# Kernel optimization log

Measured on AMD Instinct MI355X. Metric: run time of the kernel, lower is better.

The kernel has to match this reference:

```python
import jax, jax.numpy as jnp
import numpy as np

VTH = 1.0      # v_threshold
TAU = 2.0      # spikingjelly LIFNode default tau
ALPHA = 2.0    # ATan surrogate alpha
EPS = 1e-5     # BatchNorm eps
N_HEADS = 8
TOPK = 4       # routed regions per query region
REGION = 64    # tokens per region (4096 tokens -> 64 regions)


@jax.custom_vjp
def spike_fn(v):
    return (v >= VTH).astype(v.dtype)

def _spike_fwd(v):
    return (v >= VTH).astype(v.dtype), v

def _spike_bwd(v, g):
    sg = (ALPHA / 2.0) / (1.0 + (jnp.pi / 2.0 * ALPHA * (v - VTH)) ** 2)
    return (g * sg,)

spike_fn.defvjp(_spike_fwd, _spike_bwd)


def lif(x):
    # x: [T, B, L, D]; LIF with decay_input=True, hard reset to 0, detach_reset
    def step(v, xt):
        v = v + (xt - v) / TAU
        s = spike_fn(v)
        v = v * (1.0 - jax.lax.stop_gradient(s))
        return v, s
    _, s = jax.lax.scan(step, jnp.zeros_like(x[0]), x)
    return s


def batchnorm(x, gamma, beta):
    # torch BN1d over [T*B, D, L] in training mode == per-channel stats over (T,B,L)
    mean = x.mean(axis=(0, 1, 2))
    var = jnp.mean((x - mean) ** 2, axis=(0, 1, 2))
    return (x - mean) * jax.lax.rsqrt(var + EPS) * gamma + beta


def bilevel_attn(x, qkv_w, qkv_b, proj_w, proj_b):
    # x: [TB, L, D]
    TB, L, D = x.shape
    nreg = L // REGION
    hd = D // N_HEADS
    qkv = x @ qkv_w.T + qkv_b
    q, k, v = jnp.split(qkv, 3, axis=-1)
    qr = q.reshape(TB, nreg, REGION, D)
    kr = k.reshape(TB, nreg, REGION, D)
    vr = v.reshape(TB, nreg, REGION, D)
    # coarse region-level routing via mean-pooled q/k affinity
    aff = jnp.einsum('bnd,bmd->bnm', qr.mean(2), kr.mean(2))  # [TB, nreg, nreg]
    _, idx = jax.lax.top_k(aff, TOPK)                         # [TB, nreg, TOPK]
    gather = jax.vmap(lambda t, ix: t[ix])                    # per-sample region gather
    kg = gather(kr, idx).reshape(TB, nreg, TOPK * REGION, N_HEADS, hd)
    vg = gather(vr, idx).reshape(TB, nreg, TOPK * REGION, N_HEADS, hd)
    qh = qr.reshape(TB, nreg, REGION, N_HEADS, hd)
    logits = jnp.einsum('bnqhd,bnkhd->bnhqk', qh, kg) * (hd ** -0.5)
    p = jax.nn.softmax(logits, axis=-1)
    o = jnp.einsum('bnhqk,bnkhd->bnqhd', p, vg).reshape(TB, L, D)
    return o @ proj_w.T + proj_b


def setup_inputs() -> dict:
    key = jax.random.key(0)
    ks = jax.random.split(key, 8)
    T, B, Lt, L, D = 4, 2, 4, 1024, 256
    Ltot = Lt * L
    s = 0.02
    return {
        'x': jax.random.normal(ks[0], (T, B, Ltot, D), jnp.float32),
        'bn1_g': jnp.ones((D,), jnp.float32),
        'bn1_b': jnp.zeros((D,), jnp.float32),
        'bn2_g': jnp.ones((D,), jnp.float32),
        'bn2_b': jnp.zeros((D,), jnp.float32),
        'qkv_w': jax.random.normal(ks[1], (3 * D, D), jnp.float32) * s,
        'qkv_b': jnp.zeros((3 * D,), jnp.float32),
        'proj_w': jax.random.normal(ks[2], (D, D), jnp.float32) * s,
        'proj_b': jnp.zeros((D,), jnp.float32),
        'ffn_w1': jax.random.normal(ks[3], (4 * D, D), jnp.float32) * s,
        'ffn_b1': jnp.zeros((4 * D,), jnp.float32),
        'ffn_w2': jax.random.normal(ks[4], (D, 4 * D), jnp.float32) * s,
        'ffn_b2': jnp.zeros((D,), jnp.float32),
        'scale': jnp.ones((1,), jnp.float32) * 0.5,
        'Lt': Lt, 'b': B, 'L': L, 'dim': D,
    }


def reference(x, bn1_g, bn1_b, bn2_g, bn2_b, qkv_w, qkv_b, proj_w, proj_b,
              ffn_w1, ffn_b1, ffn_w2, ffn_b2, scale, Lt, b, L, dim):
    T = x.shape[0]
    Ltot = Lt * L
    # attention branch
    identity = x
    s1 = lif(batchnorm(x, bn1_g, bn1_b))
    a = bilevel_attn(s1.reshape(T * b, Ltot, dim), qkv_w, qkv_b, proj_w, proj_b)
    x = identity + a.reshape(T, b, Ltot, dim) * scale
    # ffn branch
    s2 = lif(batchnorm(x, bn2_g, bn2_b))
    h = jax.nn.gelu(s2 @ ffn_w1.T + ffn_b1, approximate=False) @ ffn_w2.T + ffn_b2
    return x + h * scale
```

## Files before the change

kernel.cpp:

```cpp
#include <hip/hip_runtime.h>
#include <hip/hip_bf16.h>
#include <math.h>

typedef __attribute__((ext_vector_type(8))) short short8;
typedef __attribute__((ext_vector_type(4))) float f32x4;

#define DIM 256
#define NROWS 32768
#define PERT 2097152
#define SAMP_TOK 4096

__device__ __forceinline__ float b2f(__hip_bfloat16 h){ return __bfloat162float(h); }
__device__ __forceinline__ __hip_bfloat16 f2b(float f){ return __float2bfloat16(f); }
__device__ __forceinline__ unsigned short f2bu(float f){
  __hip_bfloat16 h = __float2bfloat16(f);
  unsigned short u; __builtin_memcpy(&u, &h, 2); return u;
}

__global__ void f2b_k(const float* __restrict__ in, __hip_bfloat16* __restrict__ out, int n){
  int i = blockIdx.x * 256 + threadIdx.x;
  if (i < n) out[i] = f2b(in[i]);
}

__global__ void bn_stats_k(const float* __restrict__ x, float* __restrict__ sum, float* __restrict__ sumsq){
  int c = threadIdx.x;
  size_t base = (size_t)blockIdx.x * 256 * DIM + c;
  float s = 0.f, s2 = 0.f;
  for (int i = 0; i < 256; ++i){
    float v = x[base + (size_t)i * DIM];
    s += v; s2 += v * v;
  }
  atomicAdd(&sum[c], s);
  atomicAdd(&sumsq[c], s2);
}

__global__ void bn_fin_k(const float* __restrict__ sum, const float* __restrict__ sumsq,
                         const float* __restrict__ g, const float* __restrict__ b,
                         float* __restrict__ a_out, float* __restrict__ b_out){
  int c = threadIdx.x;
  float mean = sum[c] * (1.f/32768.f);
  float var  = sumsq[c] * (1.f/32768.f) - mean*mean;
  float a = g[c] / sqrtf(var + 1e-5f);
  a_out[c] = a;
  b_out[c] = b[c] - mean * a;
}

__global__ void lif_k(const float* __restrict__ x, const float* __restrict__ av,
                      const float* __restrict__ bv, __hip_bfloat16* __restrict__ s){
  int e = blockIdx.x * blockDim.x + threadIdx.x;
  if (e >= PERT) return;
  int c = e & (DIM - 1);
  float a = av[c], b = bv[c];
  float v = 0.f;
  #pragma unroll
  for (int t = 0; t < 4; ++t){
    float xn = x[(size_t)t * PERT + e] * a + b;
    v += (xn - v) * 0.5f;
    float sp = (v >= 1.0f) ? 1.0f : 0.0f;
    s[(size_t)t * PERT + e] = f2b(sp);
    v = (v >= 1.0f) ? 0.f : v;
  }
}

__global__ void region_sum_k(const __hip_bfloat16* __restrict__ s, float* __restrict__ sm){
  int r = blockIdx.x, c = threadIdx.x;
  float acc = 0.f;
  size_t base = (size_t)r * 64 * DIM + c;
  for (int i = 0; i < 64; ++i) acc += b2f(s[base + (size_t)i * DIM]);
  sm[(size_t)r * DIM + c] = acc * 0.015625f;
}

__global__ void rgemm_k(const float* __restrict__ smr, const float* __restrict__ w,
                        const float* __restrict__ bias, float* __restrict__ qkm){
  __shared__ float arow[256];
  int r = blockIdx.x, t = threadIdx.x;
  arow[t] = smr[(size_t)r * 256 + t];
  __syncthreads();
  for (int j = t; j < 512; j += 256){
    const float* wr = w + (size_t)j * 256;
    float acc = 0.f;
    for (int k = 0; k < 256; ++k) acc += arow[k] * wr[k];
    qkm[(size_t)r * 512 + j] = acc + bias[j];
  }
}

template<int EPI>
__global__ __launch_bounds__(256) void gemm_bt(
    const __hip_bfloat16* __restrict__ A, const __hip_bfloat16* __restrict__ W,
    const float* __restrict__ bias, void* __restrict__ outp,
    const void* __restrict__ extra, const float* __restrict__ scaleptr,
    int K, int N)
{
  const int LDT = 40;
  __shared__ __align__(16) short As[128 * 40];
  __shared__ __align__(16) short Ws[128 * 40];
  int tid = threadIdx.x;
  int bm = blockIdx.x, bn = blockIdx.y;
  int srow = tid >> 2;
  int scol = (tid & 3) << 3;
  int lane = tid & 63;
  int l16 = lane & 15, quad = lane >> 4;
  int wv = tid >> 6;
  int wm = (wv >> 1) << 6, wn = (wv & 1) << 6;

  f32x4 zero = {0.f, 0.f, 0.f, 0.f};
  f32x4 acc[4][4];
  #pragma unroll
  for (int i = 0; i < 4; ++i)
    #pragma unroll
    for (int j = 0; j < 4; ++j) acc[i][j] = zero;

  for (int k0 = 0; k0 < K; k0 += 32){
    #pragma unroll
    for (int p = 0; p < 2; ++p){
      int r = (p << 6) + srow;
      *reinterpret_cast<uint4*>(&As[r * LDT + scol]) =
        *reinterpret_cast<const uint4*>(A + (size_t)(bm * 128 + r) * K + k0 + scol);
      *reinterpret_cast<uint4*>(&Ws[r * LDT + scol]) =
        *reinterpret_cast<const uint4*>(W + (size_t)(bn * 128 + r) * K + k0 + scol);
    }
    __syncthreads();
    short8 af[4];
    #pragma unroll
    for (int mi = 0; mi < 4; ++mi)
      af[mi] = *reinterpret_cast<const short8*>(&As[(wm + mi * 16 + l16) * LDT + (quad << 3)]);
    #pragma unroll
    for (int ni = 0; ni < 4; ++ni){
      short8 bfr = *reinterpret_cast<const short8*>(&Ws[(wn + ni * 16 + l16) * LDT + (quad << 3)]);
      #pragma unroll
      for (int mi = 0; mi < 4; ++mi)
        acc[mi][ni] = __builtin_amdgcn_mfma_f32_16x16x32_bf16(af[mi], bfr, acc[mi][ni], 0, 0, 0);
    }
    __syncthreads();
  }

  float sc = 0.f;
  if (EPI == 1 || EPI == 3) sc = scaleptr[0];
  #pragma unroll
  for (int ni = 0; ni < 4; ++ni){
    int colg = (bn << 7) + wn + ni * 16 + l16;
    float bvl = bias[colg];
    #pragma unroll
    for (int mi = 0; mi < 4; ++mi){
      #pragma unroll
      for (int r = 0; r < 4; ++r){
        int rowg = (bm << 7) + wm + mi * 16 + (quad << 2) + r;
        float v = acc[mi][ni][r] + bvl;
        size_t off = (size_t)rowg * N + colg;
        if (EPI == 0){
          ((__hip_bfloat16*)outp)[off] = f2b(v);
        } else if (EPI == 1){
          ((float*)outp)[off] = ((const float*)extra)[off] + v * sc;
        } else if (EPI == 2){
          float gl = 0.5f * v * (1.0f + erff(v * 0.70710678118654752f));
          ((__hip_bfloat16*)outp)[off] = f2b(gl);
        } else {
          ((float*)outp)[off] = ((const float*)extra)[off] + v * sc;
        }
      }
    }
  }
}

__global__ void topk_k(const float* __restrict__ qkm, int* __restrict__ idx){
  __shared__ float aff[64];
  int r = blockIdx.x;
  int m = threadIdx.x;
  int b = r >> 6;
  const float4* qrow = reinterpret_cast<const float4*>(qkm + (size_t)r * 512);
  const float4* krow = reinterpret_cast<const float4*>(qkm + (size_t)(b * 64 + m) * 512 + 256);
  float dot = 0.f;
  for (int d = 0; d < 64; ++d){
    float4 qv = qrow[d], kv = krow[d];
    dot += qv.x * kv.x + qv.y * kv.y + qv.z * kv.z + qv.w * kv.w;
  }
  aff[m] = dot;
  __syncthreads();
  if (m == 0){
    #pragma unroll
    for (int t = 0; t < 4; ++t){
      float best = -INFINITY; int bi = 0;
      for (int i = 0; i < 64; ++i){
        if (aff[i] > best){ best = aff[i]; bi = i; }
      }
      aff[bi] = -INFINITY;
      idx[r * 4 + t] = bi;
    }
  }
}

__global__ __launch_bounds__(256) void attn_mfma_k(
    const __hip_bfloat16* __restrict__ qkv, const int* __restrict__ idx,
    __hip_bfloat16* __restrict__ o_out, int rbase)
{
  __shared__ __align__(16) short lds[27136];
  __shared__ float den_s[4][16];
  const int rl = blockIdx.x;
  const int h  = blockIdx.y;
  const int rg = rbase + rl;
  const int bl = rl >> 6;
  const int tid = threadIdx.x;
  const int w = tid >> 6, lane = tid & 63;
  const int l16 = lane & 15, quad = lane >> 4;
  short* Pw = lds + 10240 + w * 4224;

  const int reg = idx[rg * 4 + (tid >> 6)] & 63;
  const size_t srow = (size_t)bl * SAMP_TOK + (size_t)reg * 64 + (tid & 63);
  const __hip_bfloat16* kvsrc = qkv + srow * 768 + 256 + (size_t)h * 32;

  const size_t qrow = (size_t)rl * 64 + w * 16 + l16;
  short8 qf = *reinterpret_cast<const short8*>(qkv + qrow * 768 + (size_t)h * 32 + quad * 8);

  uint4 vreg[4];
  #pragma unroll
  for (int c = 0; c < 4; ++c)
    vreg[c] = *reinterpret_cast<const uint4*>(kvsrc + 256 + c * 8);

  #pragma unroll
  for (int c = 0; c < 4; ++c)
    *reinterpret_cast<uint4*>(&lds[tid * 40 + c * 8]) =
      *reinterpret_cast<const uint4*>(kvsrc + c * 8);
  __syncthreads();

  f32x4 s[16];
  #pragma unroll
  for (int nt = 0; nt < 16; ++nt){
    short8 bf = *reinterpret_cast<const short8*>(&lds[(nt * 16 + l16) * 40 + quad * 8]);
    f32x4 z = {0.f, 0.f, 0.f, 0.f};
    s[nt] = __builtin_amdgcn_mfma_f32_16x16x32_bf16(qf, bf, z, 0, 0, 0);
  }
  __syncthreads();

  #pragma unroll
  for (int c = 0; c < 4; ++c){
    short8 vv = *reinterpret_cast<short8*>(&vreg[c]);
    #pragma unroll
    for (int e = 0; e < 8; ++e)
      lds[(c * 8 + e) * 264 + tid] = vv[e];
  }

  float m4[4] = {-1e30f, -1e30f, -1e30f, -1e30f};
  #pragma unroll
  for (int nt = 0; nt < 16; ++nt)
    #pragma unroll
    for (int r = 0; r < 4; ++r) m4[r] = fmaxf(m4[r], s[nt][r]);
  #pragma unroll
  for (int xm = 1; xm < 16; xm <<= 1)
    #pragma unroll
    for (int r = 0; r < 4; ++r) m4[r] = fmaxf(m4[r], __shfl_xor(m4[r], xm));
  float d4[4] = {0.f, 0.f, 0.f, 0.f};
  #pragma unroll
  for (int nt = 0; nt < 16; ++nt)
    #pragma unroll
    for (int r = 0; r < 4; ++r){
      float e = __expf((s[nt][r] - m4[r]) * 0.17677669529663687f);
      s[nt][r] = e; d4[r] += e;
    }
  #pragma unroll
  for (int xm = 1; xm < 16; xm <<= 1)
    #pragma unroll
    for (int r = 0; r < 4; ++r) d4[r] += __shfl_xor(d4[r], xm);
  if (l16 == 0){
    #pragma unroll
    for (int r = 0; r < 4; ++r) den_s[w][quad * 4 + r] = d4[r];
  }
  #pragma unroll
  for (int nt = 0; nt < 16; ++nt)
    #pragma unroll
    for (int r = 0; r < 4; ++r)
      Pw[(quad * 4 + r) * 264 + nt * 16 + l16] = (short)f2bu(s[nt][r]);
  __syncthreads();

  f32x4 o0 = {0.f, 0.f, 0.f, 0.f}, o1 = o0;
  #pragma unroll
  for (int kk = 0; kk < 8; ++kk){
    short8 pb = *reinterpret_cast<const short8*>(&Pw[l16 * 264 + kk * 32 + quad * 8]);
    short8 a0 = *reinterpret_cast<const short8*>(&lds[l16 * 264 + kk * 32 + quad * 8]);
    short8 a1 = *reinterpret_cast<const short8*>(&lds[(16 + l16) * 264 + kk * 32 + quad * 8]);
    o0 = __builtin_amdgcn_mfma_f32_16x16x32_bf16(a0, pb, o0, 0, 0, 0);
    o1 = __builtin_amdgcn_mfma_f32_16x16x32_bf16(a1, pb, o1, 0, 0, 0);
  }
  float inv = 1.f / den_s[w][l16];
  size_t obase = ((size_t)rl * 64 + w * 16 + l16) * 256 + (size_t)h * 32;
  unsigned pk0 = (unsigned)f2bu(o0[0] * inv) | ((unsigned)f2bu(o0[1] * inv) << 16);
  unsigned pk1 = (unsigned)f2bu(o0[2] * inv) | ((unsigned)f2bu(o0[3] * inv) << 16);
  unsigned pk2 = (unsigned)f2bu(o1[0] * inv) | ((unsigned)f2bu(o1[1] * inv) << 16);
  unsigned pk3 = (unsigned)f2bu(o1[2] * inv) | ((unsigned)f2bu(o1[3] * inv) << 16);
  *reinterpret_cast<uint2*>(o_out + obase + quad * 4)      = make_uint2(pk0, pk1);
  *reinterpret_cast<uint2*>(o_out + obase + 16 + quad * 4) = make_uint2(pk2, pk3);
}

extern "C" void kernel_launch(void* const* d_in, const int* in_sizes, int n_in,
                              void* d_out, int out_size, void* d_ws, size_t ws_size,
                              hipStream_t stream)
{
  const float* x      = (const float*)d_in[0];
  const float* bn1_g  = (const float*)d_in[1];
  const float* bn1_b  = (const float*)d_in[2];
  const float* bn2_g  = (const float*)d_in[3];
  const float* bn2_b  = (const float*)d_in[4];
  const float* qkv_w  = (const float*)d_in[5];
  const float* qkv_b  = (const float*)d_in[6];
  const float* proj_w = (const float*)d_in[7];
  const float* proj_b = (const float*)d_in[8];
  const float* ffn_w1 = (const float*)d_in[9];
  const float* ffn_b1 = (const float*)d_in[10];
  const float* ffn_w2 = (const float*)d_in[11];
  const float* ffn_b2 = (const float*)d_in[12];
  const float* scale  = (const float*)d_in[13];
  float* x2 = (float*)d_out;

  char* ws = (char*)d_ws;
  const size_t MB = 1024 * 1024;
  float* sum1 = (float*)(ws + 0);
  float* sq1  = (float*)(ws + 1024);
  float* sum2 = (float*)(ws + 2048);
  float* sq2  = (float*)(ws + 3072);
  float* a1   = (float*)(ws + 4096);
  float* b1   = (float*)(ws + 5120);
  float* a2   = (float*)(ws + 6144);
  float* b2   = (float*)(ws + 7168);
  int*   idxb = (int*)(ws + 8192);
  float* smr  = (float*)(ws + 16384);
  float* qkm  = (float*)(ws + 540672);
  __hip_bfloat16* qkv_wb  = (__hip_bfloat16*)(ws + 1589248);
  __hip_bfloat16* proj_wb = (__hip_bfloat16*)(ws + 1982464);
  __hip_bfloat16* ffn_w1b = (__hip_bfloat16*)(ws + 2113536);
  __hip_bfloat16* ffn_w2b = (__hip_bfloat16*)(ws + 2637824);
  __hip_bfloat16* s1 = (__hip_bfloat16*)(ws + 4 * MB);
  __hip_bfloat16* s2 = s1;
  char* chunkbuf = ws + 20 * MB;

  size_t avail = (ws_size > 20 * MB) ? (ws_size - 20 * MB) : (8 * MB);
  int nc = (avail >= 64 * MB) ? 8 : (avail >= 32 * MB) ? 4 : (avail >= 16 * MB) ? 2 : 1;
  int crows = 32768;
  while ((size_t)crows * 2048 > avail && crows > 2048) crows >>= 1;

  __hip_bfloat16* qkvc = (__hip_bfloat16*)chunkbuf;
  __hip_bfloat16* oc   = (__hip_bfloat16*)(chunkbuf + (size_t)nc * 6 * MB);
  __hip_bfloat16* h1   = (__hip_bfloat16*)chunkbuf;

  hipMemsetAsync(d_ws, 0, 4096, stream);

  f2b_k<<<(196608 + 255) / 256, 256, 0, stream>>>(qkv_w, qkv_wb, 196608);
  f2b_k<<<(65536 + 255) / 256, 256, 0, stream>>>(proj_w, proj_wb, 65536);
  f2b_k<<<(262144 + 255) / 256, 256, 0, stream>>>(ffn_w1, ffn_w1b, 262144);
  f2b_k<<<(262144 + 255) / 256, 256, 0, stream>>>(ffn_w2, ffn_w2b, 262144);

  bn_stats_k<<<128, 256, 0, stream>>>(x, sum1, sq1);
  bn_fin_k<<<1, 256, 0, stream>>>(sum1, sq1, bn1_g, bn1_b, a1, b1);
  lif_k<<<PERT / 256, 256, 0, stream>>>(x, a1, b1, s1);
  region_sum_k<<<512, 256, 0, stream>>>(s1, smr);
  rgemm_k<<<512, 256, 0, stream>>>(smr, qkv_w, qkv_b, qkm);
  topk_k<<<512, 64, 0, stream>>>(qkm, idxb);

  const int nchunkA = 8 / nc;
  for (int c = 0; c < nchunkA; ++c){
    const size_t ro = (size_t)c * nc * SAMP_TOK;
    gemm_bt<0><<<dim3(nc * SAMP_TOK / 128, 6), 256, 0, stream>>>(
        s1 + ro * 256, qkv_wb, qkv_b, qkvc, nullptr, nullptr, 256, 768);
    attn_mfma_k<<<dim3(nc * 64, 8), 256, 0, stream>>>(qkvc, idxb, oc, c * nc * 64);
    gemm_bt<1><<<dim3(nc * SAMP_TOK / 128, 2), 256, 0, stream>>>(
        oc, proj_wb, proj_b, x2 + ro * 256, x + ro * 256, scale, 256, 256);
  }

  bn_stats_k<<<128, 256, 0, stream>>>(x2, sum2, sq2);
  bn_fin_k<<<1, 256, 0, stream>>>(sum2, sq2, bn2_g, bn2_b, a2, b2);
  lif_k<<<PERT / 256, 256, 0, stream>>>(x2, a2, b2, s2);
  const int nchunkF = 32768 / crows;
  for (int c = 0; c < nchunkF; ++c){
    const size_t ro = (size_t)c * crows;
    gemm_bt<2><<<dim3(crows / 128, 8), 256, 0, stream>>>(
        s2 + ro * 256, ffn_w1b, ffn_b1, h1, nullptr, nullptr, 256, 1024);
    gemm_bt<3><<<dim3(crows / 128, 2), 256, 0, stream>>>(
        h1, ffn_w2b, ffn_b2, x2 + ro * 256, x2 + ro * 256, scale, 1024, 256);
  }
}
```

Measured before the change: 378.5 us.

## Use direct global-to-LDS loads, vectorized epilogue, fast GELU, finer BN stats grid

The GEMM tile loads now go straight from global memory into LDS through global_load_lds, using an unpadded 32-wide layout. The MFMA operands are swapped so each lane holds four consecutive output columns, which lets the epilogue do vectorized float4 bias loads and packed bf16 or float4 stores. The exact erf GELU is replaced by a polynomial erf approximation, and the BN stats reduction is spread over 4x more blocks. The risks are LDS bank conflicts from the unpadded layout, slightly lower GELU accuracy, and more atomics in the BN reduction.

Result: slower. 399.1 us (+5.4%).

```diff
diff --git a/kernel.cpp b/kernel.cpp
--- a/kernel.cpp
+++ b/kernel.cpp
@@ -17,6 +17,22 @@
   unsigned short u; __builtin_memcpy(&u, &h, 2); return u;
 }
 
+#define GLD_LDS16(gp, lp) __builtin_amdgcn_global_load_lds( \
+    (const __attribute__((address_space(1))) unsigned int*)(gp), \
+    (__attribute__((address_space(3))) unsigned int*)(lp), 16, 0, 0)
+
+__device__ __forceinline__ float gelu_fast(float v){
+  float z  = v * 0.70710678118654752f;
+  float az = fabsf(z);
+  float t  = __builtin_amdgcn_rcpf(fmaf(0.3275911f, az, 1.0f));
+  float p  = fmaf(fmaf(fmaf(fmaf(1.061405429f, t, -1.453152027f), t,
+                            1.421413741f), t, -0.284496736f), t, 0.254829592f);
+  p *= t;
+  float e  = __expf(-z * z);
+  float y  = fmaf(-p, e, 1.0f);
+  return fmaf(0.5f * fabsf(v), y, 0.5f * v);
+}
+
 __global__ void f2b_k(const float* __restrict__ in, __hip_bfloat16* __restrict__ out, int n){
   int i = blockIdx.x * 256 + threadIdx.x;
   if (i < n) out[i] = f2b(in[i]);
@@ -24,9 +40,9 @@
 
 __global__ void bn_stats_k(const float* __restrict__ x, float* __restrict__ sum, float* __restrict__ sumsq){
   int c = threadIdx.x;
-  size_t base = (size_t)blockIdx.x * 256 * DIM + c;
+  size_t base = (size_t)blockIdx.x * 64 * DIM + c;
   float s = 0.f, s2 = 0.f;
-  for (int i = 0; i < 256; ++i){
+  for (int i = 0; i < 64; ++i){
     float v = x[base + (size_t)i * DIM];
     s += v; s2 += v * v;
   }
@@ -91,18 +107,21 @@
     const void* __restrict__ extra, const float* __restrict__ scaleptr,
     int K, int N)
 {
-  const int LDT = 40;
-  __shared__ __align__(16) short As[128 * 40];
-  __shared__ __align__(16) short Ws[128 * 40];
+  __shared__ __align__(16) short As[128 * 32];
+  __shared__ __align__(16) short Ws[128 * 32];
   int tid = threadIdx.x;
   int bm = blockIdx.x, bn = blockIdx.y;
-  int srow = tid >> 2;
-  int scol = (tid & 3) << 3;
   int lane = tid & 63;
   int l16 = lane & 15, quad = lane >> 4;
   int wv = tid >> 6;
   int wm = (wv >> 1) << 6, wn = (wv & 1) << 6;
 
+  const __hip_bfloat16* Ag = A + (size_t)(bm * 128 + (tid >> 2)) * K + ((tid & 3) << 3);
+  const __hip_bfloat16* Wg = W + (size_t)(bn * 128 + (tid >> 2)) * K + ((tid & 3) << 3);
+  short* Ad = As + tid * 8;
+  short* Wd = Ws + tid * 8;
+  const size_t rstep = (size_t)64 * K;
+
   f32x4 zero = {0.f, 0.f, 0.f, 0.f};
   f32x4 acc[4][4];
   #pragma unroll
@@ -111,52 +130,55 @@
     for (int j = 0; j < 4; ++j) acc[i][j] = zero;
 
   for (int k0 = 0; k0 < K; k0 += 32){
-    #pragma unroll
-    for (int p = 0; p < 2; ++p){
-      int r = (p << 6) + srow;
-      *reinterpret_cast<uint4*>(&As[r * LDT + scol]) =
-        *reinterpret_cast<const uint4*>(A + (size_t)(bm * 128 + r) * K + k0 + scol);
-      *reinterpret_cast<uint4*>(&Ws[r * LDT + scol]) =
-        *reinterpret_cast<const uint4*>(W + (size_t)(bn * 128 + r) * K + k0 + scol);
+    GLD_LDS16(Ag + k0,         Ad);
+    GLD_LDS16(Ag + rstep + k0, Ad + 2048);
+    GLD_LDS16(Wg + k0,         Wd);
+    GLD_LDS16(Wg + rstep + k0, Wd + 2048);
+    __syncthreads();
+    short8 af[4];
+    #pragma unroll
+    for (int mi = 0; mi < 4; ++mi)
+      af[mi] = *reinterpret_cast<const short8*>(&As[(wm + mi * 16 + l16) * 32 + (quad << 3)]);
+    #pragma unroll
+    for (int ni = 0; ni < 4; ++ni){
+      short8 wf = *reinterpret_cast<const short8*>(&Ws[(wn + ni * 16 + l16) * 32 + (quad << 3)]);
+      #pragma unroll
+      for (int mi = 0; mi < 4; ++mi)
+        acc[mi][ni] = __builtin_amdgcn_mfma_f32_16x16x32_bf16(wf, af[mi], acc[mi][ni], 0, 0, 0);
     }
     __syncthreads();
-    short8 af[4];
-    #pragma unroll
-    for (int mi = 0; mi < 4; ++mi)
-      af[mi] = *reinterpret_cast<const short8*>(&As[(wm + mi * 16 + l16) * LDT + (quad << 3)]);
-    #pragma unroll
-    for (int ni = 0; ni < 4; ++ni){
-      short8 bfr = *reinterpret_cast<const short8*>(&Ws[(wn + ni * 16 + l16) * LDT + (quad << 3)]);
-      #pragma unroll
-      for (int mi = 0; mi < 4; ++mi)
-        acc[mi][ni] = __builtin_amdgcn_mfma_f32_16x16x32_bf16(af[mi], bfr, acc[mi][ni], 0, 0, 0);
-    }
-    __syncthreads();
   }
 
   float sc = 0.f;
   if (EPI == 1 || EPI == 3) sc = scaleptr[0];
   #pragma unroll
   for (int ni = 0; ni < 4; ++ni){
-    int colg = (bn << 7) + wn + ni * 16 + l16;
-    float bvl = bias[colg];
+    int col0 = (bn << 7) + wn + ni * 16 + (quad << 2);
+    float4 bv = *reinterpret_cast<const float4*>(bias + col0);
     #pragma unroll
     for (int mi = 0; mi < 4; ++mi){
-      #pragma unroll
-      for (int r = 0; r < 4; ++r){
-        int rowg = (bm << 7) + wm + mi * 16 + (quad << 2) + r;
-        float v = acc[mi][ni][r] + bvl;
-        size_t off = (size_t)rowg * N + colg;
-        if (EPI == 0){
-          ((__hip_bfloat16*)outp)[off] = f2b(v);
-        } else if (EPI == 1){
-          ((float*)outp)[off] = ((const float*)extra)[off] + v * sc;
-        } else if (EPI == 2){
-          float gl = 0.5f * v * (1.0f + erff(v * 0.70710678118654752f));
-          ((__hip_bfloat16*)outp)[off] = f2b(gl);
-        } else {
-          ((float*)outp)[off] = ((const float*)extra)[off] + v * sc;
-        }
+      int rowg = (bm << 7) + wm + mi * 16 + l16;
+      size_t off = (size_t)rowg * N + col0;
+      float v0 = acc[mi][ni][0] + bv.x;
+      float v1 = acc[mi][ni][1] + bv.y;
+      float v2 = acc[mi][ni][2] + bv.z;
+      float v3 = acc[mi][ni][3] + bv.w;
+      if (EPI == 0){
+        unsigned lo = (unsigned)f2bu(v0) | ((unsigned)f2bu(v1) << 16);
+        unsigned hi = (unsigned)f2bu(v2) | ((unsigned)f2bu(v3) << 16);
+        *reinterpret_cast<uint2*>((__hip_bfloat16*)outp + off) = make_uint2(lo, hi);
+      } else if (EPI == 1 || EPI == 3){
+        float4 xr = *reinterpret_cast<const float4*>((const float*)extra + off);
+        float4 ov;
+        ov.x = xr.x + v0 * sc; ov.y = xr.y + v1 * sc;
+        ov.z = xr.z + v2 * sc; ov.w = xr.w + v3 * sc;
+        *reinterpret_cast<float4*>((float*)outp + off) = ov;
+      } else {
+        float g0 = gelu_fast(v0), g1 = gelu_fast(v1);
+        float g2 = gelu_fast(v2), g3 = gelu_fast(v3);
+        unsigned lo = (unsigned)f2bu(g0) | ((unsigned)f2bu(g1) << 16);
+        unsigned hi = (unsigned)f2bu(g2) | ((unsigned)f2bu(g3) << 16);
+        *reinterpret_cast<uint2*>((__hip_bfloat16*)outp + off) = make_uint2(lo, hi);
       }
     }
   }
@@ -347,7 +369,7 @@
   f2b_k<<<(262144 + 255) / 256, 256, 0, stream>>>(ffn_w1, ffn_w1b, 262144);
   f2b_k<<<(262144 + 255) / 256, 256, 0, stream>>>(ffn_w2, ffn_w2b, 262144);
 
-  bn_stats_k<<<128, 256, 0, stream>>>(x, sum1, sq1);
+  bn_stats_k<<<512, 256, 0, stream>>>(x, sum1, sq1);
   bn_fin_k<<<1, 256, 0, stream>>>(sum1, sq1, bn1_g, bn1_b, a1, b1);
   lif_k<<<PERT / 256, 256, 0, stream>>>(x, a1, b1, s1);
   region_sum_k<<<512, 256, 0, stream>>>(s1, smr);
@@ -364,7 +386,7 @@
         oc, proj_wb, proj_b, x2 + ro * 256, x + ro * 256, scale, 256, 256);
   }
 
-  bn_stats_k<<<128, 256, 0, stream>>>(x2, sum2, sq2);
+  bn_stats_k<<<512, 256, 0, stream>>>(x2, sum2, sq2);
   bn_fin_k<<<1, 256, 0, stream>>>(sum2, sq2, bn2_g, bn2_b, a2, b2);
   lif_k<<<PERT / 256, 256, 0, stream>>>(x2, a2, b2, s2);
   const int nchunkF = 32768 / crows;
```
